# Performance work log

Hardware: AMD Instinct MI355X
Metric: run time of the kernel (lower is better)

## Reference

```python
import jax, jax.numpy as jnp
import numpy as np

N_NODES = 100000
N_EDGES = 1600000
IN_FEATS, HIDDEN_FEATS, OUT_FEATS = 32, 64, 16


def setup_inputs() -> dict:
    key = jax.random.key(0)
    ks = jax.random.split(key, 8)
    return {
        "features": jax.random.normal(ks[0], (N_NODES, IN_FEATS), dtype=jnp.float32),
        "src": jax.random.randint(ks[1], (N_EDGES,), 0, N_NODES, dtype=jnp.int64),
        "dst": jax.random.randint(ks[2], (N_EDGES,), 0, N_NODES, dtype=jnp.int64),
        "W1_self": jax.random.normal(ks[3], (IN_FEATS, HIDDEN_FEATS), dtype=jnp.float32) * 0.1,
        "W1_neigh": jax.random.normal(ks[4], (IN_FEATS, HIDDEN_FEATS), dtype=jnp.float32) * 0.1,
        "b1": jnp.zeros((HIDDEN_FEATS,), dtype=jnp.float32),
        "W2_self": jax.random.normal(ks[5], (HIDDEN_FEATS, OUT_FEATS), dtype=jnp.float32) * 0.1,
        "W2_neigh": jax.random.normal(ks[6], (HIDDEN_FEATS, OUT_FEATS), dtype=jnp.float32) * 0.1,
        "b2": jnp.zeros((OUT_FEATS,), dtype=jnp.float32),
    }


def _sage_conv_mean(h, src, dst, n_nodes, W_self, W_neigh, b):
    # DGL SAGEConv(mean): gather src features to edges, mean-reduce at dst,
    # then fc_self(h) + fc_neigh(mean_neigh) + bias.
    ones = jnp.ones(src.shape, dtype=h.dtype)
    deg = jax.ops.segment_sum(ones, dst, num_segments=n_nodes)  # in-degree [N]
    agg = jax.ops.segment_sum(h[src], dst, num_segments=n_nodes)  # [N, d]
    mean_neigh = agg / jnp.maximum(deg, 1.0)[:, None]
    return h @ W_self + mean_neigh @ W_neigh + b


def reference(features, src, dst, W1_self, W1_neigh, b1, W2_self, W2_neigh, b2):
    n = features.shape[0]
    h = _sage_conv_mean(features, src, dst, n, W1_self, W1_neigh, b1)
    h = jax.nn.relu(h)
    # dropout is identity at inference (Keras call default training=False)
    out = _sage_conv_mean(h, src, dst, n, W2_self, W2_neigh, b2)
    return out
```

## Files before the change

### kernel.cpp

```cpp
#include <hip/hip_runtime.h>

#define N_NODES 100000
#define N_EDGES 1600000
#define IN_F 32
#define HID_F 64
#define OUT_F 16
#define BSIZE 512
#define NBKT 256
#define CAP 10240
#define CHUNK 4096
#define NBUCK ((N_NODES + BSIZE - 1) / BSIZE)
#define APITCH 68

using f2v = __attribute__((ext_vector_type(2))) float;

__device__ __forceinline__ unsigned f2bf(float f) {
  unsigned u = __float_as_uint(f);
  return (u + 0x7FFFu + ((u >> 16) & 1u)) >> 16;
}

#define ADDQ(s, Q) do { f2v p_; \
  p_ = __builtin_amdgcn_cvt_pk_f32_fp8((int)(Q).x, false); s[0] += p_[0]; s[1] += p_[1]; \
  p_ = __builtin_amdgcn_cvt_pk_f32_fp8((int)(Q).x, true);  s[2] += p_[0]; s[3] += p_[1]; \
  p_ = __builtin_amdgcn_cvt_pk_f32_fp8((int)(Q).y, false); s[4] += p_[0]; s[5] += p_[1]; \
  p_ = __builtin_amdgcn_cvt_pk_f32_fp8((int)(Q).y, true);  s[6] += p_[0]; s[7] += p_[1]; \
  p_ = __builtin_amdgcn_cvt_pk_f32_fp8((int)(Q).z, false); s[8] += p_[0]; s[9] += p_[1]; \
  p_ = __builtin_amdgcn_cvt_pk_f32_fp8((int)(Q).z, true);  s[10] += p_[0]; s[11] += p_[1]; \
  p_ = __builtin_amdgcn_cvt_pk_f32_fp8((int)(Q).w, false); s[12] += p_[0]; s[13] += p_[1]; \
  p_ = __builtin_amdgcn_cvt_pk_f32_fp8((int)(Q).w, true);  s[14] += p_[0]; s[15] += p_[1]; \
} while (0)

__global__ __launch_bounds__(NBKT) void cursor_init_kernel(int* __restrict__ cursor) {
  cursor[threadIdx.x] = threadIdx.x * CAP;
}

__global__ __launch_bounds__(512) void bucket_kernel(
    const int* __restrict__ src, const int* __restrict__ dst,
    int* __restrict__ cursor, unsigned* __restrict__ sorted) {
  __shared__ unsigned stage[CHUNK];
  __shared__ unsigned char sbkt[CHUNK];
  __shared__ int lcnt[NBKT], lscan[NBKT], gbase[NBKT];
  int t = threadIdx.x;
  if (t < NBKT) lcnt[t] = 0;
  __syncthreads();

  int base = blockIdx.x * CHUNK;
  unsigned mypk[CHUNK / 512];
  int myb[CHUNK / 512], myrank[CHUNK / 512];
#pragma unroll
  for (int i = 0; i < CHUNK / 512; ++i) {
    int e = base + t + 512 * i;
    if (e < N_EDGES) {
      unsigned s = (unsigned)src[e], d = (unsigned)dst[e];
      myb[i] = (int)(d >> 9);
      mypk[i] = (s << 9) | (d & 511u);
      myrank[i] = atomicAdd(&lcnt[myb[i]], 1);
    } else {
      myb[i] = -1;
    }
  }
  __syncthreads();
  if (t < NBKT) lscan[t] = lcnt[t];
  __syncthreads();
  for (int off = 1; off < NBKT; off <<= 1) {
    int v = (t < NBKT && t >= off) ? lscan[t - off] : 0;
    __syncthreads();
    if (t < NBKT) lscan[t] += v;
    __syncthreads();
  }
  if (t < NBKT) gbase[t] = lcnt[t] ? atomicAdd(&cursor[t], lcnt[t]) : 0;
  __syncthreads();
#pragma unroll
  for (int i = 0; i < CHUNK / 512; ++i) {
    if (myb[i] >= 0) {
      int slot = (lscan[myb[i]] - lcnt[myb[i]]) + myrank[i];
      stage[slot] = mypk[i];
      sbkt[slot] = (unsigned char)myb[i];
    }
  }
  __syncthreads();
  int nvalid = min(CHUNK, N_EDGES - base);
  for (int i = t; i < nvalid; i += 512) {
    unsigned p = stage[i];
    int b = (int)sbkt[i];
    int addr = gbase[b] + (i - (lscan[b] - lcnt[b]));
    sorted[addr] = p;
  }
}

__global__ __launch_bounds__(1024) void bcsr_kernel(
    const unsigned* __restrict__ sorted, const int* __restrict__ cursor,
    const float4* __restrict__ featin, int* __restrict__ ptr,
    int* __restrict__ col, uint4* __restrict__ featfp8) {
  __shared__ int lcnt[BSIZE];
  __shared__ int lcur[BSIZE];
  __shared__ int scanbuf[BSIZE];
  int t = threadIdx.x;
  int b = blockIdx.x;

  {
    int gtid = b * 1024 + t;
    if (gtid < N_NODES * IN_F / 16) {
      float4 a = featin[4 * gtid], bb = featin[4 * gtid + 1];
      float4 c4 = featin[4 * gtid + 2], d = featin[4 * gtid + 3];
      uint4 r;
      int w;
      w = __builtin_amdgcn_cvt_pk_fp8_f32(a.x, a.y, 0, false);
      w = __builtin_amdgcn_cvt_pk_fp8_f32(a.z, a.w, w, true);
      r.x = (unsigned)w;
      w = __builtin_amdgcn_cvt_pk_fp8_f32(bb.x, bb.y, 0, false);
      w = __builtin_amdgcn_cvt_pk_fp8_f32(bb.z, bb.w, w, true);
      r.y = (unsigned)w;
      w = __builtin_amdgcn_cvt_pk_fp8_f32(c4.x, c4.y, 0, false);
      w = __builtin_amdgcn_cvt_pk_fp8_f32(c4.z, c4.w, w, true);
      r.z = (unsigned)w;
      w = __builtin_amdgcn_cvt_pk_fp8_f32(d.x, d.y, 0, false);
      w = __builtin_amdgcn_cvt_pk_fp8_f32(d.z, d.w, w, true);
      r.w = (unsigned)w;
      featfp8[gtid] = r;
    }
  }

  int base = b * CAP;
  int ne = cursor[b] - base;

  if (t < BSIZE) lcnt[t] = 0;
  __syncthreads();
  for (int i = t; i < ne; i += 1024)
    atomicAdd(&lcnt[sorted[base + i] & (BSIZE - 1)], 1);
  __syncthreads();

  int c = 0;
  if (t < BSIZE) { c = lcnt[t]; scanbuf[t] = c; }
  __syncthreads();
  for (int off = 1; off < BSIZE; off <<= 1) {
    int u = (t < BSIZE && t >= off) ? scanbuf[t - off] : 0;
    __syncthreads();
    if (t < BSIZE) scanbuf[t] += u;
    __syncthreads();
  }
  if (t < BSIZE) {
    int incl = scanbuf[t];
    lcur[t] = base + incl - c;
    int v = b * BSIZE + t;
    if (v < N_NODES) ptr[v] = base + incl;
  }
  __syncthreads();

  for (int i = t; i < ne; i += 1024) {
    unsigned p = sorted[base + i];
    int pos = atomicAdd(&lcur[p & (BSIZE - 1)], 1);
    col[pos] = (int)(p >> 9);
  }
}

__global__ __launch_bounds__(256) void l1g_kernel(
    const float* __restrict__ feat, const uint4* __restrict__ featfp8,
    const int* __restrict__ ptr, const int* __restrict__ col,
    const float* __restrict__ W1s, const float* __restrict__ W1n,
    const float* __restrict__ b1,
    const float* __restrict__ W2n, const float* __restrict__ W2s,
    unsigned* __restrict__ t2f8, float* __restrict__ s2) {
  __shared__ float sA[64 * APITCH];
  __shared__ float sW[64 * 64];

  int t = threadIdx.x;
  int tile = blockIdx.x * 64;
  int nvalid = min(64, N_NODES - tile);

  if (t < 128) {
    int c = t & 1, nl = t >> 1;
    int v = tile + nl;
    if (nl < nvalid) {
      int start = (v & (BSIZE - 1)) ? ptr[v - 1] : (v >> 9) * CAP;
      int end = ptr[v];
      float s[16];
#pragma unroll
      for (int j = 0; j < 16; ++j) s[j] = 0.0f;
      int e = start;
      for (; e + 3 < end; e += 4) {
        uint4 q0 = featfp8[col[e] * 2 + c];
        uint4 q1 = featfp8[col[e + 1] * 2 + c];
        uint4 q2 = featfp8[col[e + 2] * 2 + c];
        uint4 q3 = featfp8[col[e + 3] * 2 + c];
        ADDQ(s, q0);
        ADDQ(s, q1);
        ADDQ(s, q2);
        ADDQ(s, q3);
      }
      for (; e < end; ++e) {
        uint4 q = featfp8[col[e] * 2 + c];
        ADDQ(s, q);
      }
      float inv = 1.0f / fmaxf((float)(end - start), 1.0f);
#pragma unroll
      for (int j = 0; j < 16; ++j)
        sA[(32 + 16 * c + j) * APITCH + nl] = s[j] * inv;
    }
  } else {
    int u = t - 128;
    const float4* Fg = (const float4*)(feat + (size_t)tile * IN_F);
    int lim = nvalid * 8;
#pragma unroll
    for (int it = 0; it < 4; ++it) {
      int idx = u + 128 * it;
      int n = idx >> 3, c = idx & 7;
      if (idx < lim) {
        float4 a = Fg[idx];
        sA[(4 * c + 0) * APITCH + n] = a.x;
        sA[(4 * c + 1) * APITCH + n] = a.y;
        sA[(4 * c + 2) * APITCH + n] = a.z;
        sA[(4 * c + 3) * APITCH + n] = a.w;
      }
    }
    float4* Ws = (float4*)sW;
#pragma unroll
    for (int it = 0; it < 8; ++it) {
      int idx = u + 128 * it;
      int row = idx >> 4;
      const float4* srcw = (row < 32) ? (const float4*)W1s : (const float4*)W1n;
      Ws[idx] = srcw[(row & 31) * 16 + (idx & 15)];
    }
  }
  int tx = t & 15, ty = t >> 4;
  int n0 = 4 * ty, c0 = 4 * tx;
  float4 bb = ((const float4*)b1)[tx];
  __syncthreads();

  float acc[4][4];
#pragma unroll
  for (int i = 0; i < 4; ++i) { acc[i][0] = bb.x; acc[i][1] = bb.y; acc[i][2] = bb.z; acc[i][3] = bb.w; }
#pragma unroll 4
  for (int k = 0; k < 64; ++k) {
    float4 a = *(const float4*)&sA[k * APITCH + n0];
    float4 w = *(const float4*)&sW[k * 64 + c0];
    acc[0][0] += a.x * w.x; acc[0][1] += a.x * w.y; acc[0][2] += a.x * w.z; acc[0][3] += a.x * w.w;
    acc[1][0] += a.y * w.x; acc[1][1] += a.y * w.y; acc[1][2] += a.y * w.z; acc[1][3] += a.y * w.w;
    acc[2][0] += a.z * w.x; acc[2][1] += a.z * w.y; acc[2][2] += a.z * w.z; acc[2][3] += a.z * w.w;
    acc[3][0] += a.w * w.x; acc[3][1] += a.w * w.y; acc[3][2] += a.w * w.z; acc[3][3] += a.w * w.w;
  }
  __syncthreads();

#pragma unroll
  for (int jj = 0; jj < 4; ++jj) {
    float4 v;
    v.x = fmaxf(acc[0][jj], 0.0f);
    v.y = fmaxf(acc[1][jj], 0.0f);
    v.z = fmaxf(acc[2][jj], 0.0f);
    v.w = fmaxf(acc[3][jj], 0.0f);
    *(float4*)&sA[(c0 + jj) * APITCH + n0] = v;
  }
  {
    float4* Ws = (float4*)sW;
#pragma unroll
    for (int it = 0; it < 2; ++it) {
      int idx = t + 256 * it;
      int row = idx >> 3, ch = idx & 7;
      const float4* srcw = (ch < 4) ? (const float4*)W2n : (const float4*)W2s;
      Ws[row * 8 + ch] = srcw[row * 4 + (ch & 3)];
    }
  }
  __syncthreads();

  int c2 = 2 * tx;
  float a0 = 0.f, a1 = 0.f, b0 = 0.f, b1_ = 0.f, d0 = 0.f, d1 = 0.f, e0 = 0.f, e1 = 0.f;
#pragma unroll 4
  for (int k = 0; k < 64; ++k) {
    float4 a = *(const float4*)&sA[k * APITCH + n0];
    float2 w = *(const float2*)&sW[k * 32 + c2];
    a0 += a.x * w.x; a1 += a.x * w.y;
    b0 += a.y * w.x; b1_ += a.y * w.y;
    d0 += a.z * w.x; d1 += a.z * w.y;
    e0 += a.w * w.x; e1 += a.w * w.y;
  }
  {
    float rs[4][2] = {{a0, a1}, {b0, b1_}, {d0, d1}, {e0, e1}};
    int cc = c2 & 15;
#pragma unroll
    for (int i = 0; i < 4; ++i) {
      int v = tile + n0 + i;
      if (v < N_NODES) {
        if (c2 < 16) {
          int w = __builtin_amdgcn_cvt_pk_fp8_f32(rs[i][0], rs[i][1], 0, false);
          *(unsigned short*)((char*)t2f8 + (size_t)v * 16 + cc) = (unsigned short)w;
        } else {
          *(float2*)&s2[v * OUT_F + cc] = make_float2(rs[i][0], rs[i][1]);
        }
      }
    }
  }
}

__global__ __launch_bounds__(256) void gather2_final_kernel(
    const int* __restrict__ ptr, const int* __restrict__ col,
    const uint4* __restrict__ t2f8, const float* __restrict__ s2,
    const float* __restrict__ b2, float* __restrict__ out) {
  int v = blockIdx.x * 256 + threadIdx.x;
  if (v >= N_NODES) return;
  int start = (v & (BSIZE - 1)) ? ptr[v - 1] : (v >> 9) * CAP;
  int end = ptr[v];
  float s[16];
#pragma unroll
  for (int j = 0; j < 16; ++j) s[j] = 0.0f;
  int e = start;
  for (; e + 3 < end; e += 4) {
    uint4 q0 = t2f8[col[e]];
    uint4 q1 = t2f8[col[e + 1]];
    uint4 q2 = t2f8[col[e + 2]];
    uint4 q3 = t2f8[col[e + 3]];
    ADDQ(s, q0);
    ADDQ(s, q1);
    ADDQ(s, q2);
    ADDQ(s, q3);
  }
  for (; e < end; ++e) {
    uint4 q = t2f8[col[e]];
    ADDQ(s, q);
  }
  float inv = 1.0f / fmaxf((float)(end - start), 1.0f);
  const float4* S = (const float4*)s2;
  const float4* B = (const float4*)b2;
  float4* O = (float4*)out;
#pragma unroll
  for (int i = 0; i < 4; ++i) {
    float4 sv = S[v * 4 + i];
    float4 bv = B[i];
    float4 r;
    r.x = sv.x + bv.x + s[4 * i + 0] * inv;
    r.y = sv.y + bv.y + s[4 * i + 1] * inv;
    r.z = sv.z + bv.z + s[4 * i + 2] * inv;
    r.w = sv.w + bv.w + s[4 * i + 3] * inv;
    O[v * 4 + i] = r;
  }
}

extern "C" void kernel_launch(void* const* d_in, const int* in_sizes, int n_in,
                              void* d_out, int out_size, void* d_ws, size_t ws_size,
                              hipStream_t stream) {
  const float* feat = (const float*)d_in[0];
  const int* src    = (const int*)d_in[1];
  const int* dst    = (const int*)d_in[2];
  const float* W1s  = (const float*)d_in[3];
  const float* W1n  = (const float*)d_in[4];
  const float* b1   = (const float*)d_in[5];
  const float* W2s  = (const float*)d_in[6];
  const float* W2n  = (const float*)d_in[7];
  const float* b2   = (const float*)d_in[8];
  float* out = (float*)d_out;

  const size_t N = N_NODES;
  const size_t SLAB = (size_t)NBKT * CAP;
  int* ptr = (int*)d_ws;
  int* col = ptr + N + 8;
  unsigned* sorted = (unsigned*)(col + SLAB);
  float* s2 = (float*)(sorted + SLAB);
  unsigned* featfp8 = (unsigned*)(s2 + 16 * N);
  unsigned* t2f8 = featfp8 + 8 * N;
  int* cursor = (int*)(t2f8 + 4 * N);

  cursor_init_kernel<<<1, NBKT, 0, stream>>>(cursor);
  bucket_kernel<<<(N_EDGES + CHUNK - 1) / CHUNK, 512, 0, stream>>>(src, dst, cursor, sorted);
  bcsr_kernel<<<NBUCK, 1024, 0, stream>>>(sorted, cursor, (const float4*)feat,
                                          ptr, col, (uint4*)featfp8);
  l1g_kernel<<<(N_NODES + 63) / 64, 256, 0, stream>>>(
      feat, (const uint4*)featfp8, ptr, col, W1s, W1n, b1, W2n, W2s, t2f8, s2);
  gather2_final_kernel<<<(N_NODES + 255) / 256, 256, 0, stream>>>(
      ptr, col, (const uint4*)t2f8, s2, b2, out);
}
```

Measured before the change: 165.1 us.

## Split neighbor gathers across thread pairs and cache edges in registers during CSR build

```diff
diff --git a/kernel.cpp b/kernel.cpp
--- a/kernel.cpp
+++ b/kernel.cpp
@@ -93,7 +93,6 @@
     const float4* __restrict__ featin, int* __restrict__ ptr,
     int* __restrict__ col, uint4* __restrict__ featfp8) {
   __shared__ int lcnt[BSIZE];
-  __shared__ int lcur[BSIZE];
   __shared__ int scanbuf[BSIZE];
   int t = threadIdx.x;
   int b = blockIdx.x;
@@ -126,12 +125,24 @@
 
   if (t < BSIZE) lcnt[t] = 0;
   __syncthreads();
-  for (int i = t; i < ne; i += 1024)
-    atomicAdd(&lcnt[sorted[base + i] & (BSIZE - 1)], 1);
-  __syncthreads();
-
-  int c = 0;
-  if (t < BSIZE) { c = lcnt[t]; scanbuf[t] = c; }
+
+  int myd[CAP / 1024], myr[CAP / 1024];
+  unsigned mysrc[CAP / 1024];
+#pragma unroll
+  for (int j = 0; j < CAP / 1024; ++j) {
+    int i = t + 1024 * j;
+    myd[j] = -1;
+    if (i < ne) {
+      unsigned p = sorted[base + i];
+      int d = (int)(p & (BSIZE - 1));
+      mysrc[j] = p >> 9;
+      myd[j] = d;
+      myr[j] = atomicAdd(&lcnt[d], 1);
+    }
+  }
+  __syncthreads();
+
+  if (t < BSIZE) scanbuf[t] = lcnt[t];
   __syncthreads();
   for (int off = 1; off < BSIZE; off <<= 1) {
     int u = (t < BSIZE && t >= off) ? scanbuf[t - off] : 0;
@@ -140,17 +151,17 @@
     __syncthreads();
   }
   if (t < BSIZE) {
-    int incl = scanbuf[t];
-    lcur[t] = base + incl - c;
-    int v = b * BSIZE + t;
-    if (v < N_NODES) ptr[v] = base + incl;
-  }
-  __syncthreads();
-
-  for (int i = t; i < ne; i += 1024) {
-    unsigned p = sorted[base + i];
-    int pos = atomicAdd(&lcur[p & (BSIZE - 1)], 1);
-    col[pos] = (int)(p >> 9);
+    int vtx = b * BSIZE + t;
+    if (vtx < N_NODES) ptr[vtx] = base + scanbuf[t];
+  }
+  __syncthreads();
+
+#pragma unroll
+  for (int j = 0; j < CAP / 1024; ++j) {
+    if (myd[j] >= 0) {
+      int d = myd[j];
+      col[base + scanbuf[d] - lcnt[d] + myr[j]] = (int)mysrc[j];
+    }
   }
 }
 
@@ -168,8 +179,23 @@
   int tile = blockIdx.x * 64;
   int nvalid = min(64, N_NODES - tile);
 
-  if (t < 128) {
-    int c = t & 1, nl = t >> 1;
+  const float4* Fg = (const float4*)(feat + (size_t)tile * IN_F);
+  int lim = nvalid * 8;
+  int fi0 = t, fi1 = t + 256;
+  float4 fa0, fa1;
+  if (fi0 < lim) fa0 = Fg[fi0];
+  if (fi1 < lim) fa1 = Fg[fi1];
+  float4 wv[4];
+#pragma unroll
+  for (int it = 0; it < 4; ++it) {
+    int idx = t + 256 * it;
+    int row = idx >> 4;
+    const float4* srcw = (row < 32) ? (const float4*)W1s : (const float4*)W1n;
+    wv[it] = srcw[(row & 31) * 16 + (idx & 15)];
+  }
+
+  {
+    int nl = t >> 2, c = (t >> 1) & 1, hp = t & 1;
     int v = tile + nl;
     if (nl < nvalid) {
       int start = (v & (BSIZE - 1)) ? ptr[v - 1] : (v >> 9) * CAP;
@@ -177,51 +203,51 @@
       float s[16];
 #pragma unroll
       for (int j = 0; j < 16; ++j) s[j] = 0.0f;
-      int e = start;
-      for (; e + 3 < end; e += 4) {
+      int e = start + hp;
+      for (; e + 6 < end; e += 8) {
         uint4 q0 = featfp8[col[e] * 2 + c];
-        uint4 q1 = featfp8[col[e + 1] * 2 + c];
-        uint4 q2 = featfp8[col[e + 2] * 2 + c];
-        uint4 q3 = featfp8[col[e + 3] * 2 + c];
+        uint4 q1 = featfp8[col[e + 2] * 2 + c];
+        uint4 q2 = featfp8[col[e + 4] * 2 + c];
+        uint4 q3 = featfp8[col[e + 6] * 2 + c];
         ADDQ(s, q0);
         ADDQ(s, q1);
         ADDQ(s, q2);
         ADDQ(s, q3);
       }
-      for (; e < end; ++e) {
+      for (; e < end; e += 2) {
         uint4 q = featfp8[col[e] * 2 + c];
         ADDQ(s, q);
       }
+#pragma unroll
+      for (int j = 0; j < 16; ++j) s[j] += __shfl_xor(s[j], 1);
       float inv = 1.0f / fmaxf((float)(end - start), 1.0f);
-#pragma unroll
-      for (int j = 0; j < 16; ++j)
-        sA[(32 + 16 * c + j) * APITCH + nl] = s[j] * inv;
-    }
-  } else {
-    int u = t - 128;
-    const float4* Fg = (const float4*)(feat + (size_t)tile * IN_F);
-    int lim = nvalid * 8;
-#pragma unroll
-    for (int it = 0; it < 4; ++it) {
-      int idx = u + 128 * it;
-      int n = idx >> 3, c = idx & 7;
-      if (idx < lim) {
-        float4 a = Fg[idx];
-        sA[(4 * c + 0) * APITCH + n] = a.x;
-        sA[(4 * c + 1) * APITCH + n] = a.y;
-        sA[(4 * c + 2) * APITCH + n] = a.z;
-        sA[(4 * c + 3) * APITCH + n] = a.w;
-      }
-    }
+      int j0 = 8 * hp;
+#pragma unroll
+      for (int j = 0; j < 8; ++j)
+        sA[(32 + 16 * c + j0 + j) * APITCH + nl] = s[j0 + j] * inv;
+    }
+  }
+
+  if (fi0 < lim) {
+    int n = fi0 >> 3, c8 = fi0 & 7;
+    sA[(4 * c8 + 0) * APITCH + n] = fa0.x;
+    sA[(4 * c8 + 1) * APITCH + n] = fa0.y;
+    sA[(4 * c8 + 2) * APITCH + n] = fa0.z;
+    sA[(4 * c8 + 3) * APITCH + n] = fa0.w;
+  }
+  if (fi1 < lim) {
+    int n = fi1 >> 3, c8 = fi1 & 7;
+    sA[(4 * c8 + 0) * APITCH + n] = fa1.x;
+    sA[(4 * c8 + 1) * APITCH + n] = fa1.y;
+    sA[(4 * c8 + 2) * APITCH + n] = fa1.z;
+    sA[(4 * c8 + 3) * APITCH + n] = fa1.w;
+  }
+  {
     float4* Ws = (float4*)sW;
 #pragma unroll
-    for (int it = 0; it < 8; ++it) {
-      int idx = u + 128 * it;
-      int row = idx >> 4;
-      const float4* srcw = (row < 32) ? (const float4*)W1s : (const float4*)W1n;
-      Ws[idx] = srcw[(row & 31) * 16 + (idx & 15)];
-    }
-  }
+    for (int it = 0; it < 4; ++it) Ws[t + 256 * it] = wv[it];
+  }
+
   int tx = t & 15, ty = t >> 4;
   int n0 = 4 * ty, c0 = 4 * tx;
   float4 bb = ((const float4*)b1)[tx];
@@ -295,42 +321,46 @@
     const int* __restrict__ ptr, const int* __restrict__ col,
     const uint4* __restrict__ t2f8, const float* __restrict__ s2,
     const float* __restrict__ b2, float* __restrict__ out) {
-  int v = blockIdx.x * 256 + threadIdx.x;
+  int g = blockIdx.x * 256 + threadIdx.x;
+  int v = g >> 1, hp = g & 1;
   if (v >= N_NODES) return;
   int start = (v & (BSIZE - 1)) ? ptr[v - 1] : (v >> 9) * CAP;
   int end = ptr[v];
   float s[16];
 #pragma unroll
   for (int j = 0; j < 16; ++j) s[j] = 0.0f;
-  int e = start;
-  for (; e + 3 < end; e += 4) {
+  int e = start + hp;
+  for (; e + 6 < end; e += 8) {
     uint4 q0 = t2f8[col[e]];
-    uint4 q1 = t2f8[col[e + 1]];
-    uint4 q2 = t2f8[col[e + 2]];
-    uint4 q3 = t2f8[col[e + 3]];
+    uint4 q1 = t2f8[col[e + 2]];
+    uint4 q2 = t2f8[col[e + 4]];
+    uint4 q3 = t2f8[col[e + 6]];
     ADDQ(s, q0);
     ADDQ(s, q1);
     ADDQ(s, q2);
     ADDQ(s, q3);
   }
-  for (; e < end; ++e) {
+  for (; e < end; e += 2) {
     uint4 q = t2f8[col[e]];
     ADDQ(s, q);
   }
+#pragma unroll
+  for (int j = 0; j < 16; ++j) s[j] += __shfl_xor(s[j], 1);
   float inv = 1.0f / fmaxf((float)(end - start), 1.0f);
   const float4* S = (const float4*)s2;
   const float4* B = (const float4*)b2;
   float4* O = (float4*)out;
 #pragma unroll
-  for (int i = 0; i < 4; ++i) {
-    float4 sv = S[v * 4 + i];
-    float4 bv = B[i];
+  for (int i = 0; i < 2; ++i) {
+    int ii = 2 * hp + i;
+    float4 sv = S[v * 4 + ii];
+    float4 bv = B[ii];
     float4 r;
-    r.x = sv.x + bv.x + s[4 * i + 0] * inv;
-    r.y = sv.y + bv.y + s[4 * i + 1] * inv;
-    r.z = sv.z + bv.z + s[4 * i + 2] * inv;
-    r.w = sv.w + bv.w + s[4 * i + 3] * inv;
-    O[v * 4 + i] = r;
+    r.x = sv.x + bv.x + s[4 * ii + 0] * inv;
+    r.y = sv.y + bv.y + s[4 * ii + 1] * inv;
+    r.z = sv.z + bv.z + s[4 * ii + 2] * inv;
+    r.w = sv.w + bv.w + s[4 * ii + 3] * inv;
+    O[v * 4 + ii] = r;
   }
 }
 
@@ -364,6 +394,6 @@
                                           ptr, col, (uint4*)featfp8);
   l1g_kernel<<<(N_NODES + 63) / 64, 256, 0, stream>>>(
       feat, (const uint4*)featfp8, ptr, col, W1s, W1n, b1, W2n, W2s, t2f8, s2);
-  gather2_final_kernel<<<(N_NODES + 255) / 256, 256, 0, stream>>>(
+  gather2_final_kernel<<<(2 * N_NODES + 255) / 256, 256, 0, stream>>>(
       ptr, col, (const uint4*)t2f8, s2, b2, out);
 }
```

Measured after the change: 167.1 us. Within noise of the previous version (+1.2%).
